# Kernel tuning notes

Measured on AMD Instinct MI355X. Metric: run time of the kernel, lower is better.

Reference implementation:

```python
import jax, jax.numpy as jnp
import numpy as np

B, S, DIM, N, D = 1, 2688, 1536, 12, 128
C = D // 2  # 64 complex pairs per head
EPS = 1e-06


def rms_norm(x, g, eps=EPS):
    # x: [B, S, DIM] -- norm over full model dim, as in WanRMSNorm
    xf = x.astype(jnp.float32)
    return (xf * jax.lax.rsqrt(jnp.mean(xf * xf, axis=-1, keepdims=True) + eps)) * g


def rope_apply(x, f, h, w, freqs_c):
    # x: [B, S, N, D]; freqs_c: complex64 [1024, C]; f*h*w == S (full-seq case)
    s1 = C - 2 * (C // 3)  # 22 (temporal)
    s2 = C // 3            # 21 (height), 21 (width)
    ff = freqs_c[:f, :s1]
    fh = freqs_c[:h, s1:s1 + s2]
    fw = freqs_c[:w, s1 + s2:]
    fi = jnp.concatenate([
        jnp.broadcast_to(ff[:, None, None, :], (f, h, w, s1)),
        jnp.broadcast_to(fh[None, :, None, :], (f, h, w, s2)),
        jnp.broadcast_to(fw[None, None, :, :], (f, h, w, s2)),
    ], axis=-1).reshape(f * h * w, 1, C)  # [S, 1, C]
    xr = x.astype(jnp.float32).reshape(B, S, N, C, 2)
    xc = jax.lax.complex(xr[..., 0], xr[..., 1])          # [B, S, N, C]
    out = xc * fi[None]                                    # broadcast over B, N
    return jnp.stack([out.real, out.imag], axis=-1).reshape(B, S, N, D)


def setup_inputs() -> dict:
    key = jax.random.key(0)
    ks = jax.random.split(key, 12)
    w_scale = 0.02
    # deterministic rope angles (faithful structure: exp(i*theta) per axis slice)
    pos = np.arange(1024, dtype=np.float32)
    inv = 1.0 / (10000.0 ** (np.arange(C, dtype=np.float32) / C))
    ang = pos[:, None] * inv[None, :]
    return {
        "x": jax.random.normal(ks[0], (B, S, DIM), jnp.float32),
        "seq_lens": jnp.full((B,), S, dtype=jnp.int32),
        "grid_sizes": jnp.array([[6, 16, 28]], dtype=jnp.int32),
        "freqs_cos": jnp.asarray(np.cos(ang), jnp.float32),
        "freqs_sin": jnp.asarray(np.sin(ang), jnp.float32),
        "Wq": jax.random.normal(ks[1], (DIM, DIM), jnp.float32) * w_scale,
        "bq": jnp.zeros((DIM,), jnp.float32),
        "Wk": jax.random.normal(ks[2], (DIM, DIM), jnp.float32) * w_scale,
        "bk": jnp.zeros((DIM,), jnp.float32),
        "Wv": jax.random.normal(ks[3], (DIM, DIM), jnp.float32) * w_scale,
        "bv": jnp.zeros((DIM,), jnp.float32),
        "Wo": jax.random.normal(ks[4], (DIM, DIM), jnp.float32) * w_scale,
        "bo": jnp.zeros((DIM,), jnp.float32),
        "gq": jnp.ones((DIM,), jnp.float32),
        "gk": jnp.ones((DIM,), jnp.float32),
    }


def reference(x, seq_lens, grid_sizes, freqs_cos, freqs_sin,
              Wq, bq, Wk, bk, Wv, bv, Wo, bo, gq, gk):
    f, h, w = (int(grid_sizes[0, 0]), int(grid_sizes[0, 1]), int(grid_sizes[0, 2]))
    freqs_c = jax.lax.complex(freqs_cos, freqs_sin)  # [1024, C]

    q = rms_norm(x @ Wq.T + bq, gq).reshape(B, S, N, D)
    k = rms_norm(x @ Wk.T + bk, gk).reshape(B, S, N, D)
    v = (x @ Wv.T + bv).reshape(B, S, N, D)

    q = rope_apply(q, f, h, w, freqs_c)
    k = rope_apply(k, f, h, w, freqs_c)

    # SDPA with key-length masking (k_lens)
    scale = 1.0 / jnp.sqrt(jnp.float32(D))
    scores = jnp.einsum("bqnd,bknd->bnqk", q, k) * scale  # [B, N, S, S]
    kmask = jnp.arange(S)[None, :] < seq_lens[:, None]     # [B, S]
    scores = jnp.where(kmask[:, None, None, :], scores, -jnp.inf)
    attn = jax.nn.softmax(scores, axis=-1)
    out = jnp.einsum("bnqk,bknd->bqnd", attn, v).reshape(B, S, DIM)
    return out @ Wo.T + bo
```

## Files before the change

### kernel.cpp

```cpp
#include <hip/hip_runtime.h>
#include <hip/hip_bf16.h>
#include <stdint.h>

#define S_LEN 2688
#define DIM   1536
#define NH    12
#define HD    128
#define QKV_N 4608

typedef __attribute__((ext_vector_type(8))) short bf16x8;
typedef __attribute__((ext_vector_type(4))) float f32x4;

__device__ inline ushort f2bf(float f) {
    uint32_t u = __float_as_uint(f);
    uint32_t r = (u + 0x7fffu + ((u >> 16) & 1u)) >> 16;
    return (ushort)r;
}
__device__ inline float bf2f(uint u) { return __uint_as_float(u << 16); }
__device__ inline float fexp2(float x) {
    float r;
    asm("v_exp_f32 %0, %1" : "=v"(r) : "v"(x));
    return r;
}
__device__ inline uint cvtpk(float lo, float hi) {
    uint r;
    asm("v_cvt_pk_bf16_f32 %0, %1, %2" : "=v"(r) : "v"(lo), "v"(hi));
    return r;
}

#define GLOAD16(gp, lp) __builtin_amdgcn_global_load_lds( \
    (__attribute__((address_space(1))) const void*)(gp),  \
    (__attribute__((address_space(3))) void*)(lp), 16, 0, 0)

__global__ __launch_bounds__(256) void convert_all(
    const float* __restrict__ x,
    const float* __restrict__ wq, const float* __restrict__ wk,
    const float* __restrict__ wv, const float* __restrict__ wo,
    ushort* __restrict__ xb, ushort* __restrict__ wb)
{
    const size_t NX4 = (size_t)S_LEN * DIM / 4;
    const size_t NW4 = (size_t)DIM * DIM / 4;
    size_t i = (size_t)blockIdx.x * 256 + threadIdx.x;
    const float* src; ushort* dst;
    if (i < NX4)            { src = x;  dst = xb; }
    else if (i < NX4+1*NW4) { src = wq; dst = wb;                        i -= NX4; }
    else if (i < NX4+2*NW4) { src = wk; dst = wb + 1*(size_t)DIM*DIM;    i -= NX4+1*NW4; }
    else if (i < NX4+3*NW4) { src = wv; dst = wb + 2*(size_t)DIM*DIM;    i -= NX4+2*NW4; }
    else if (i < NX4+4*NW4) { src = wo; dst = wb + 3*(size_t)DIM*DIM;    i -= NX4+3*NW4; }
    else return;
    float4 v = reinterpret_cast<const float4*>(src)[i];
    ushort4 o = { f2bf(v.x), f2bf(v.y), f2bf(v.z), f2bf(v.w) };
    reinterpret_cast<ushort4*>(dst)[i] = o;
}

__global__ __launch_bounds__(256) void gemm_qkv(
    const ushort* __restrict__ A, const ushort* __restrict__ B,
    const float* __restrict__ bq, const float* __restrict__ bk,
    const float* __restrict__ bv,
    ushort* __restrict__ qkb, ushort* __restrict__ v_t, int K)
{
    __shared__ ushort At[128 * 64];
    __shared__ ushort Bt[128 * 64];
    const int tid  = threadIdx.x;
    const int wave = tid >> 6, lane = tid & 63;
    const int lid  = blockIdx.y * 21 + blockIdx.x;
    const int xcd  = lid & 7, pos = lid >> 3;
    const int wgid = (xcd < 4 ? xcd * 95 : 4 * 95 + (xcd - 4) * 94) + pos;
    const int m0 = (wgid % 21) * 128, n0 = (wgid / 21) * 128;
    const int wr = wave >> 1, wc = wave & 1;
    const int r = lane & 15, g = lane >> 4;
    const int srow = wave * 8 + (lane >> 3);
    const int scol = (lane & 7) * 8;

    f32x4 acc[4][4] = {};

    for (int k0 = 0; k0 < K; k0 += 64) {
        const ushort* Ag = A + (size_t)m0 * K + k0;
        const ushort* Bg = B + (size_t)n0 * K + k0;
#pragma unroll
        for (int t = 0; t < 4; ++t) {
            GLOAD16(Ag + (size_t)(t*32 + srow) * K + scol, &At[t*2048 + wave*512]);
            GLOAD16(Bg + (size_t)(t*32 + srow) * K + scol, &Bt[t*2048 + wave*512]);
        }
        asm volatile("s_waitcnt vmcnt(0)" ::: "memory");
        __syncthreads();
#pragma unroll
        for (int kk = 0; kk < 2; ++kk) {
            bf16x8 af[4], bfr[4];
#pragma unroll
            for (int i = 0; i < 4; ++i)
                af[i] = *reinterpret_cast<const bf16x8*>(
                    &At[(wr*64 + i*16 + r) * 64 + kk*32 + g*8]);
#pragma unroll
            for (int i = 0; i < 4; ++i)
                bfr[i] = *reinterpret_cast<const bf16x8*>(
                    &Bt[(wc*64 + i*16 + r) * 64 + kk*32 + g*8]);
#pragma unroll
            for (int mi = 0; mi < 4; ++mi)
#pragma unroll
                for (int ni = 0; ni < 4; ++ni)
                    acc[mi][ni] = __builtin_amdgcn_mfma_f32_16x16x32_bf16(
                        af[mi], bfr[ni], acc[mi][ni], 0, 0, 0);
        }
        __syncthreads();
    }

    if (n0 < 2*DIM) {
#pragma unroll
        for (int ni = 0; ni < 4; ++ni) {
            int col = n0 + wc*64 + ni*16 + r;
            float bias = (col < DIM) ? bq[col] : bk[col - DIM];
#pragma unroll
            for (int mi = 0; mi < 4; ++mi) {
                int row = m0 + wr*64 + mi*16 + g*4;
#pragma unroll
                for (int j = 0; j < 4; ++j)
                    qkb[(size_t)(row + j) * (2*DIM) + col] =
                        f2bf(acc[mi][ni][j] + bias);
            }
        }
    } else {
#pragma unroll
        for (int ni = 0; ni < 4; ++ni) {
            int d = n0 - 2*DIM + wc*64 + ni*16 + r;
            float bias = bv[d];
#pragma unroll
            for (int mi = 0; mi < 4; ++mi) {
                int row = m0 + wr*64 + mi*16 + g*4;
                uint2 pkt;
                pkt.x = cvtpk(acc[mi][ni][0] + bias, acc[mi][ni][1] + bias);
                pkt.y = cvtpk(acc[mi][ni][2] + bias, acc[mi][ni][3] + bias);
                *reinterpret_cast<uint2*>(&v_t[(size_t)d * S_LEN + row]) = pkt;
            }
        }
    }
}

__global__ __launch_bounds__(256) void gemm_bt2(
    const ushort* __restrict__ A, const ushort* __restrict__ B,
    const float* __restrict__ b0,
    float* __restrict__ C, int M, int N, int K)
{
    __shared__ ushort At[128 * 64];
    __shared__ ushort Bt[64 * 64];
    const int tid  = threadIdx.x;
    const int wave = tid >> 6, lane = tid & 63;
    const int m0 = blockIdx.x * 128, n0 = blockIdx.y * 64;
    const int wr = wave >> 1, wc = wave & 1;
    const int r = lane & 15, g = lane >> 4;
    const int srow = wave * 8 + (lane >> 3);
    const int scol = (lane & 7) * 8;
    const int brow[2] = { (0*256+tid)>>3, (1*256+tid)>>3 };
    const int bcol = (tid & 7) * 8;

    f32x4 acc[4][2] = {};

    for (int k0 = 0; k0 < K; k0 += 64) {
        const ushort* Ag = A + (size_t)m0 * K + k0;
        const ushort* Bg = B + (size_t)n0 * K + k0;
#pragma unroll
        for (int t = 0; t < 4; ++t)
            GLOAD16(Ag + (size_t)(t*32 + srow) * K + scol, &At[t*2048 + wave*512]);
#pragma unroll
        for (int t = 0; t < 2; ++t)
            GLOAD16(Bg + (size_t)brow[t] * K + bcol, &Bt[(t*256 + wave*64) * 8]);
        asm volatile("s_waitcnt vmcnt(0)" ::: "memory");
        __syncthreads();
#pragma unroll
        for (int kk = 0; kk < 2; ++kk) {
            bf16x8 af[4], bfr[2];
#pragma unroll
            for (int i = 0; i < 4; ++i)
                af[i] = *reinterpret_cast<const bf16x8*>(
                    &At[(wr*64 + i*16 + r) * 64 + kk*32 + g*8]);
#pragma unroll
            for (int i = 0; i < 2; ++i)
                bfr[i] = *reinterpret_cast<const bf16x8*>(
                    &Bt[(wc*32 + i*16 + r) * 64 + kk*32 + g*8]);
#pragma unroll
            for (int mi = 0; mi < 4; ++mi)
#pragma unroll
                for (int ni = 0; ni < 2; ++ni)
                    acc[mi][ni] = __builtin_amdgcn_mfma_f32_16x16x32_bf16(
                        af[mi], bfr[ni], acc[mi][ni], 0, 0, 0);
        }
        __syncthreads();
    }

#pragma unroll
    for (int ni = 0; ni < 2; ++ni) {
        int col = n0 + wc*32 + ni*16 + r;
        float bias = b0[col];
#pragma unroll
        for (int mi = 0; mi < 4; ++mi) {
            int row = m0 + wr*64 + mi*16 + g*4;
#pragma unroll
            for (int j = 0; j < 4; ++j)
                C[(size_t)(row + j) * N + col] = acc[mi][ni][j] + bias;
        }
    }
}

__global__ __launch_bounds__(256) void normrope(
    const ushort* __restrict__ qkb, const int* __restrict__ gsz,
    const float* __restrict__ gq, const float* __restrict__ gk,
    const float* __restrict__ fcos, const float* __restrict__ fsin,
    ushort* __restrict__ q_r, ushort* __restrict__ k_r)
{
    const int s   = blockIdx.x;
    const int tid = threadIdx.x;
    const int wave = tid >> 6, lane = tid & 63;
    const uint* qrow = reinterpret_cast<const uint*>(qkb + (size_t)s * (2*DIM));
    const uint* krow = qrow + DIM/2;

    float2 qv[3], kv[3];
    float sq = 0.f, sk = 0.f;
#pragma unroll
    for (int i = 0; i < 3; ++i) {
        int p = tid + i*256;
        uint uq = qrow[p], uk = krow[p];
        qv[i].x = bf2f(uq & 0xffffu); qv[i].y = bf2f(uq >> 16);
        kv[i].x = bf2f(uk & 0xffffu); kv[i].y = bf2f(uk >> 16);
        sq += qv[i].x*qv[i].x + qv[i].y*qv[i].y;
        sk += kv[i].x*kv[i].x + kv[i].y*kv[i].y;
    }
#pragma unroll
    for (int off = 1; off < 64; off <<= 1) {
        sq += __shfl_xor(sq, off);
        sk += __shfl_xor(sk, off);
    }
    __shared__ float red[4][2];
    if (lane == 0) { red[wave][0] = sq; red[wave][1] = sk; }
    __syncthreads();
    sq = red[0][0] + red[1][0] + red[2][0] + red[3][0];
    sk = red[0][1] + red[1][1] + red[2][1] + red[3][1];
    const float rmsq = rsqrtf(sq * (1.f/DIM) + 1e-6f);
    const float rmsk = rsqrtf(sk * (1.f/DIM) + 1e-6f);

    const int hh = gsz[1], ww = gsz[2];
    const int fidx = s / (hh*ww), rem = s % (hh*ww);
    const int hidx = rem / ww,  widx = rem % ww;
    const float qscale = rmsq * (0.08838834764831845f * 1.4426950408889634f);

#pragma unroll
    for (int i = 0; i < 3; ++i) {
        int p = tid + i*256;
        int c = p & 63, head = p >> 6;
        int coord = (c < 22) ? fidx : (c < 43) ? hidx : widx;
        float cv = fcos[coord*64 + c], sv = fsin[coord*64 + c];
        float2 gqv = reinterpret_cast<const float2*>(gq)[p];
        float2 gkv = reinterpret_cast<const float2*>(gk)[p];
        float a = qv[i].x * qscale * gqv.x, b = qv[i].y * qscale * gqv.y;
        uint qo = cvtpk(a*cv - b*sv, a*sv + b*cv);
        a = kv[i].x * rmsk * gkv.x; b = kv[i].y * rmsk * gkv.y;
        uint ko = cvtpk(a*cv - b*sv, a*sv + b*cv);
        size_t off = (((size_t)head * S_LEN + s) * HD + 2*c) >> 1;
        reinterpret_cast<uint*>(q_r)[off] = qo;
        reinterpret_cast<uint*>(k_r)[off] = ko;
    }
}

__global__ __launch_bounds__(256) void attn_fwd(
    const ushort* __restrict__ q_r, const ushort* __restrict__ k_r,
    const ushort* __restrict__ v_t, const int* __restrict__ seq_lens,
    ushort* __restrict__ attn_out)
{
    __shared__ ushort Kl[2][64 * 128];
    __shared__ ushort Vl[2][128 * 64];
    __shared__ ushort Pl[4][16 * 72];
    const int tid  = threadIdx.x;
    const int wave = tid >> 6, lane = tid & 63;
    const int n  = blockIdx.y;
    const int q0 = blockIdx.x * 64 + wave * 16;
    const int seq = seq_lens[0];
    const int r = lane & 15, g = lane >> 4;
    const int swz = r & 7;
    const ushort* Qh = q_r + (size_t)n * S_LEN * HD;
    const ushort* Kh = k_r + (size_t)n * S_LEN * HD;
    const ushort* Vh = v_t + (size_t)n * HD * S_LEN;

    const int kj_row[4] = { (0*256+tid)>>4, (1*256+tid)>>4, (2*256+tid)>>4, (3*256+tid)>>4 };
    const int kj_w  = tid & 15;
    const int vj_d[4]  = { (0*256+tid)>>3, (1*256+tid)>>3, (2*256+tid)>>3, (3*256+tid)>>3 };
    const int vj_w  = tid & 7;

    bf16x8 qf[4];
#pragma unroll
    for (int c = 0; c < 4; ++c)
        qf[c] = *reinterpret_cast<const bf16x8*>(Qh + (size_t)(q0 + r) * HD + c*32 + g*8);

    f32x4 oacc[8] = {};
    float mrun = -1e30f, lrun = 0.f;

    const int nt = (seq + 63) >> 6;

#define STAGE(buf, kbase)                                                     \
    do {                                                                      \
        _Pragma("unroll")                                                     \
        for (int t = 0; t < 4; ++t) {                                         \
            int row = kj_row[t];                                              \
            GLOAD16(Kh + (size_t)((kbase) + row) * HD + ((kj_w ^ (row & 7)) * 8), \
                    &Kl[buf][(t*256 + wave*64) * 8]);                         \
        }                                                                     \
        _Pragma("unroll")                                                     \
        for (int t = 0; t < 4; ++t) {                                         \
            int d = vj_d[t];                                                  \
            GLOAD16(Vh + (size_t)d * S_LEN + (kbase) + ((vj_w ^ (d & 7)) * 8), \
                    &Vl[buf][(t*256 + wave*64) * 8]);                         \
        }                                                                     \
    } while (0)

    STAGE(0, 0);
    asm volatile("s_waitcnt vmcnt(0)" ::: "memory");
    __syncthreads();

    int cur = 0;
    for (int kt = 0; kt < nt; ++kt) {
        const int k0 = kt * 64;
        if (kt + 1 < nt) STAGE(cur ^ 1, k0 + 64);

        f32x4 sf[4];
#pragma unroll
        for (int kb = 0; kb < 4; ++kb) {
            f32x4 s = {0.f, 0.f, 0.f, 0.f};
            const ushort* kl = &Kl[cur][(kb*16 + r) * 128];
#pragma unroll
            for (int c = 0; c < 4; ++c)
                s = __builtin_amdgcn_mfma_f32_16x16x32_bf16(
                    *reinterpret_cast<const bf16x8*>(kl + ((4*c + g) ^ swz) * 8),
                    qf[c], s, 0, 0, 0);
            sf[kb] = s;
        }
        if (k0 + 64 > seq) {
#pragma unroll
            for (int kb = 0; kb < 4; ++kb)
#pragma unroll
                for (int j = 0; j < 4; ++j)
                    if (k0 + kb*16 + g*4 + j >= seq) sf[kb][j] = -1e30f;
        }
        float pm = fmaxf(fmaxf(fmaxf(sf[0][0], sf[0][1]), fmaxf(sf[0][2], sf[0][3])),
                         fmaxf(fmaxf(sf[1][0], sf[1][1]), fmaxf(sf[1][2], sf[1][3])));
        pm = fmaxf(pm, fmaxf(fmaxf(fmaxf(sf[2][0], sf[2][1]), fmaxf(sf[2][2], sf[2][3])),
                             fmaxf(fmaxf(sf[3][0], sf[3][1]), fmaxf(sf[3][2], sf[3][3]))));
        pm = fmaxf(pm, __shfl_xor(pm, 16));
        pm = fmaxf(pm, __shfl_xor(pm, 32));
        if (!__all(pm - mrun <= 8.f)) {
            float mn = fmaxf(mrun, pm);
            float scl = fexp2(mrun - mn);
            mrun = mn;
            lrun *= scl;
#pragma unroll
            for (int f = 0; f < 8; ++f)
#pragma unroll
                for (int j = 0; j < 4; ++j) oacc[f][j] *= scl;
        }
        float ps = 0.f;
#pragma unroll
        for (int kb = 0; kb < 4; ++kb) {
            float e0 = fexp2(sf[kb][0] - mrun), e1 = fexp2(sf[kb][1] - mrun);
            float e2 = fexp2(sf[kb][2] - mrun), e3 = fexp2(sf[kb][3] - mrun);
            sf[kb][0] = e0; sf[kb][1] = e1; sf[kb][2] = e2; sf[kb][3] = e3;
            ps += (e0 + e1) + (e2 + e3);
        }
        ps += __shfl_xor(ps, 16);
        ps += __shfl_xor(ps, 32);
        lrun += ps;
#pragma unroll
        for (int kb = 0; kb < 4; ++kb) {
            uint2 pkt;
            pkt.x = cvtpk(sf[kb][0], sf[kb][1]);
            pkt.y = cvtpk(sf[kb][2], sf[kb][3]);
            *reinterpret_cast<uint2*>(&Pl[wave][r*72 + kb*16 + g*4]) = pkt;
        }
        bf16x8 pf[2];
        pf[0] = *reinterpret_cast<const bf16x8*>(&Pl[wave][r*72 + g*8]);
        pf[1] = *reinterpret_cast<const bf16x8*>(&Pl[wave][r*72 + 32 + g*8]);
#pragma unroll
        for (int db = 0; db < 8; ++db) {
            const ushort* vl = &Vl[cur][(db*16 + r) * 64];
#pragma unroll
            for (int kb2 = 0; kb2 < 2; ++kb2)
                oacc[db] = __builtin_amdgcn_mfma_f32_16x16x32_bf16(
                    *reinterpret_cast<const bf16x8*>(vl + ((kb2*4 + g) ^ swz) * 8),
                    pf[kb2], oacc[db], 0, 0, 0);
        }

        if (kt + 1 < nt) {
            asm volatile("s_waitcnt vmcnt(0)" ::: "memory");
            __syncthreads();
            cur ^= 1;
        }
    }
#undef STAGE

    const float inv = (lrun > 0.f) ? 1.f / lrun : 0.f;
#pragma unroll
    for (int db = 0; db < 8; ++db) {
        uint2 pkt;
        pkt.x = cvtpk(oacc[db][0]*inv, oacc[db][1]*inv);
        pkt.y = cvtpk(oacc[db][2]*inv, oacc[db][3]*inv);
        *reinterpret_cast<uint2*>(
            &attn_out[(size_t)(q0 + r) * DIM + n*HD + db*16 + g*4]) = pkt;
    }
}

extern "C" void kernel_launch(void* const* d_in, const int* in_sizes, int n_in,
                              void* d_out, int out_size, void* d_ws, size_t ws_size,
                              hipStream_t stream)
{
    const float* x    = (const float*)d_in[0];
    const int*   seqL = (const int*)  d_in[1];
    const int*   gsz  = (const int*)  d_in[2];
    const float* fcos = (const float*)d_in[3];
    const float* fsin = (const float*)d_in[4];
    const float* Wq   = (const float*)d_in[5];
    const float* bq   = (const float*)d_in[6];
    const float* Wk   = (const float*)d_in[7];
    const float* bk   = (const float*)d_in[8];
    const float* Wv   = (const float*)d_in[9];
    const float* bv   = (const float*)d_in[10];
    const float* Wo   = (const float*)d_in[11];
    const float* bo   = (const float*)d_in[12];
    const float* gq   = (const float*)d_in[13];
    const float* gk   = (const float*)d_in[14];
    float* out = (float*)d_out;

    char* ws = (char*)d_ws;
    ushort* xb  = (ushort*)ws;
    ushort* wb  = xb  + (size_t)S_LEN * DIM;
    ushort* qkb = wb  + 4*(size_t)DIM*DIM;
    ushort* v_t = qkb + (size_t)S_LEN * 2*DIM;
    ushort* q_r = v_t + (size_t)DIM * S_LEN;
    ushort* k_r = q_r + (size_t)S_LEN * DIM;
    ushort* ao  = k_r + (size_t)S_LEN * DIM;

    convert_all<<<13248, 256, 0, stream>>>(x, Wq, Wk, Wv, Wo, xb, wb);
    gemm_qkv<<<dim3(21, 36), 256, 0, stream>>>(xb, wb, bq, bk, bv,
                                               qkb, v_t, DIM);
    normrope<<<S_LEN, 256, 0, stream>>>(qkb, gsz, gq, gk, fcos, fsin, q_r, k_r);
    attn_fwd<<<dim3(42, 12), 256, 0, stream>>>(q_r, k_r, v_t, seqL, ao);
    gemm_bt2<<<dim3(21, 24), 256, 0, stream>>>(ao, wb + 3*(size_t)DIM*DIM,
                                               bo, out, S_LEN, DIM, DIM);
}
```

Before: 216.9 us.

## Use 32x32x16 MFMA with split-K waves and permlane P exchange

Reworks the attention kernel so each wave pair shares 32 query rows. Each wave of the pair handles one 32-key half of every 64-key tile using 32x32x16 bf16 MFMAs. The P tile is rearranged in registers with v_permlane32_swap instead of a round trip through LDS. The two halves' softmax states and output accumulators are merged through shared memory at the end. This cuts LDS traffic and the count of MFMA instructions, at the cost of a final cross-wave reduction and larger per-thread register use.

Result: faster. 208.8 us (-3.8%).

```diff
diff --git a/kernel.cpp b/kernel.cpp
--- a/kernel.cpp
+++ b/kernel.cpp
@@ -8,8 +8,9 @@
 #define HD    128
 #define QKV_N 4608
 
-typedef __attribute__((ext_vector_type(8))) short bf16x8;
-typedef __attribute__((ext_vector_type(4))) float f32x4;
+typedef __attribute__((ext_vector_type(8)))  short bf16x8;
+typedef __attribute__((ext_vector_type(4)))  float f32x4;
+typedef __attribute__((ext_vector_type(16))) float f32x16;
 
 __device__ inline ushort f2bf(float f) {
     uint32_t u = __float_as_uint(f);
@@ -267,14 +268,13 @@
 {
     __shared__ ushort Kl[2][64 * 128];
     __shared__ ushort Vl[2][128 * 64];
-    __shared__ ushort Pl[4][16 * 72];
     const int tid  = threadIdx.x;
     const int wave = tid >> 6, lane = tid & 63;
     const int n  = blockIdx.y;
-    const int q0 = blockIdx.x * 64 + wave * 16;
     const int seq = seq_lens[0];
-    const int r = lane & 15, g = lane >> 4;
-    const int swz = r & 7;
+    const int khalf = wave & 1, pair = wave >> 1;
+    const int ql = lane & 31, h = lane >> 5, sw = lane & 7;
+    const int qrow = blockIdx.x * 64 + pair * 32 + ql;
     const ushort* Qh = q_r + (size_t)n * S_LEN * HD;
     const ushort* Kh = k_r + (size_t)n * S_LEN * HD;
     const ushort* Vh = v_t + (size_t)n * HD * S_LEN;
@@ -284,12 +284,12 @@
     const int vj_d[4]  = { (0*256+tid)>>3, (1*256+tid)>>3, (2*256+tid)>>3, (3*256+tid)>>3 };
     const int vj_w  = tid & 7;
 
-    bf16x8 qf[4];
-#pragma unroll
-    for (int c = 0; c < 4; ++c)
-        qf[c] = *reinterpret_cast<const bf16x8*>(Qh + (size_t)(q0 + r) * HD + c*32 + g*8);
-
-    f32x4 oacc[8] = {};
+    bf16x8 qf[8];
+#pragma unroll
+    for (int c = 0; c < 8; ++c)
+        qf[c] = *reinterpret_cast<const bf16x8*>(Qh + (size_t)qrow * HD + c*16 + h*8);
+
+    f32x16 oacc[4] = {};
     float mrun = -1e30f, lrun = 0.f;
 
     const int nt = (seq + 63) >> 6;
@@ -316,33 +316,24 @@
 
     int cur = 0;
     for (int kt = 0; kt < nt; ++kt) {
-        const int k0 = kt * 64;
-        if (kt + 1 < nt) STAGE(cur ^ 1, k0 + 64);
-
-        f32x4 sf[4];
-#pragma unroll
-        for (int kb = 0; kb < 4; ++kb) {
-            f32x4 s = {0.f, 0.f, 0.f, 0.f};
-            const ushort* kl = &Kl[cur][(kb*16 + r) * 128];
-#pragma unroll
-            for (int c = 0; c < 4; ++c)
-                s = __builtin_amdgcn_mfma_f32_16x16x32_bf16(
-                    *reinterpret_cast<const bf16x8*>(kl + ((4*c + g) ^ swz) * 8),
-                    qf[c], s, 0, 0, 0);
-            sf[kb] = s;
-        }
-        if (k0 + 64 > seq) {
-#pragma unroll
-            for (int kb = 0; kb < 4; ++kb)
-#pragma unroll
-                for (int j = 0; j < 4; ++j)
-                    if (k0 + kb*16 + g*4 + j >= seq) sf[kb][j] = -1e30f;
-        }
-        float pm = fmaxf(fmaxf(fmaxf(sf[0][0], sf[0][1]), fmaxf(sf[0][2], sf[0][3])),
-                         fmaxf(fmaxf(sf[1][0], sf[1][1]), fmaxf(sf[1][2], sf[1][3])));
-        pm = fmaxf(pm, fmaxf(fmaxf(fmaxf(sf[2][0], sf[2][1]), fmaxf(sf[2][2], sf[2][3])),
-                             fmaxf(fmaxf(sf[3][0], sf[3][1]), fmaxf(sf[3][2], sf[3][3]))));
-        pm = fmaxf(pm, __shfl_xor(pm, 16));
+        const int k0 = kt * 64 + khalf * 32;
+        if (kt + 1 < nt) STAGE(cur ^ 1, (kt+1) * 64);
+
+        f32x16 sf = {};
+        const ushort* kl = &Kl[cur][(khalf*32 + ql) * 128];
+#pragma unroll
+        for (int c = 0; c < 8; ++c)
+            sf = __builtin_amdgcn_mfma_f32_32x32x16_bf16(
+                *reinterpret_cast<const bf16x8*>(kl + ((2*c + h) ^ sw) * 8),
+                qf[c], sf, 0, 0, 0);
+        if (k0 + 32 > seq) {
+#pragma unroll
+            for (int j = 0; j < 16; ++j)
+                if (k0 + (j&3) + 8*(j>>2) + 4*h >= seq) sf[j] = -1e30f;
+        }
+        float pm = sf[0];
+#pragma unroll
+        for (int j = 1; j < 16; ++j) pm = fmaxf(pm, sf[j]);
         pm = fmaxf(pm, __shfl_xor(pm, 32));
         if (!__all(pm - mrun <= 8.f)) {
             float mn = fmaxf(mrun, pm);
@@ -350,39 +341,39 @@
             mrun = mn;
             lrun *= scl;
 #pragma unroll
-            for (int f = 0; f < 8; ++f)
-#pragma unroll
-                for (int j = 0; j < 4; ++j) oacc[f][j] *= scl;
+            for (int db = 0; db < 4; ++db)
+#pragma unroll
+                for (int j = 0; j < 16; ++j) oacc[db][j] *= scl;
         }
         float ps = 0.f;
 #pragma unroll
-        for (int kb = 0; kb < 4; ++kb) {
-            float e0 = fexp2(sf[kb][0] - mrun), e1 = fexp2(sf[kb][1] - mrun);
-            float e2 = fexp2(sf[kb][2] - mrun), e3 = fexp2(sf[kb][3] - mrun);
-            sf[kb][0] = e0; sf[kb][1] = e1; sf[kb][2] = e2; sf[kb][3] = e3;
-            ps += (e0 + e1) + (e2 + e3);
-        }
-        ps += __shfl_xor(ps, 16);
+        for (int j = 0; j < 16; ++j) {
+            float e = fexp2(sf[j] - mrun);
+            sf[j] = e;
+            ps += e;
+        }
         ps += __shfl_xor(ps, 32);
         lrun += ps;
-#pragma unroll
-        for (int kb = 0; kb < 4; ++kb) {
-            uint2 pkt;
-            pkt.x = cvtpk(sf[kb][0], sf[kb][1]);
-            pkt.y = cvtpk(sf[kb][2], sf[kb][3]);
-            *reinterpret_cast<uint2*>(&Pl[wave][r*72 + kb*16 + g*4]) = pkt;
-        }
-        bf16x8 pf[2];
-        pf[0] = *reinterpret_cast<const bf16x8*>(&Pl[wave][r*72 + g*8]);
-        pf[1] = *reinterpret_cast<const bf16x8*>(&Pl[wave][r*72 + 32 + g*8]);
-#pragma unroll
-        for (int db = 0; db < 8; ++db) {
-            const ushort* vl = &Vl[cur][(db*16 + r) * 64];
-#pragma unroll
-            for (int kb2 = 0; kb2 < 2; ++kb2)
-                oacc[db] = __builtin_amdgcn_mfma_f32_16x16x32_bf16(
-                    *reinterpret_cast<const bf16x8*>(vl + ((kb2*4 + g) ^ swz) * 8),
-                    pf[kb2], oacc[db], 0, 0, 0);
+        uint u0 = cvtpk(sf[0],  sf[1]),  u1 = cvtpk(sf[2],  sf[3]);
+        uint u2 = cvtpk(sf[4],  sf[5]),  u3 = cvtpk(sf[6],  sf[7]);
+        uint u4 = cvtpk(sf[8],  sf[9]),  u5 = cvtpk(sf[10], sf[11]);
+        uint u6 = cvtpk(sf[12], sf[13]), u7 = cvtpk(sf[14], sf[15]);
+        asm("v_permlane32_swap_b32 %0, %1" : "+v"(u0), "+v"(u2));
+        asm("v_permlane32_swap_b32 %0, %1" : "+v"(u1), "+v"(u3));
+        asm("v_permlane32_swap_b32 %0, %1" : "+v"(u4), "+v"(u6));
+        asm("v_permlane32_swap_b32 %0, %1" : "+v"(u5), "+v"(u7));
+        union { uint uu[4]; bf16x8 v; } fa, fb;
+        fa.uu[0] = u0; fa.uu[1] = u1; fa.uu[2] = u2; fa.uu[3] = u3;
+        fb.uu[0] = u4; fb.uu[1] = u5; fb.uu[2] = u6; fb.uu[3] = u7;
+#pragma unroll
+        for (int db = 0; db < 4; ++db) {
+            const ushort* vl = &Vl[cur][(db*32 + ql) * 64];
+            oacc[db] = __builtin_amdgcn_mfma_f32_32x32x16_bf16(
+                *reinterpret_cast<const bf16x8*>(vl + ((khalf*4 + 0 + h) ^ sw) * 8),
+                fa.v, oacc[db], 0, 0, 0);
+            oacc[db] = __builtin_amdgcn_mfma_f32_32x32x16_bf16(
+                *reinterpret_cast<const bf16x8*>(vl + ((khalf*4 + 2 + h) ^ sw) * 8),
+                fb.v, oacc[db], 0, 0, 0);
         }
 
         if (kt + 1 < nt) {
@@ -393,14 +384,44 @@
     }
 #undef STAGE
 
-    const float inv = (lrun > 0.f) ? 1.f / lrun : 0.f;
-#pragma unroll
-    for (int db = 0; db < 8; ++db) {
-        uint2 pkt;
-        pkt.x = cvtpk(oacc[db][0]*inv, oacc[db][1]*inv);
-        pkt.y = cvtpk(oacc[db][2]*inv, oacc[db][3]*inv);
-        *reinterpret_cast<uint2*>(
-            &attn_out[(size_t)(q0 + r) * DIM + n*HD + db*16 + g*4]) = pkt;
+    __syncthreads();
+    float* Obuf  = (float*)&Kl[0][0];
+    float* MLbuf = (float*)&Vl[0][0];
+    if (khalf == 1) {
+#pragma unroll
+        for (int db = 0; db < 4; ++db)
+#pragma unroll
+            for (int j = 0; j < 16; ++j) {
+                int d = db*32 + (j&3) + 8*(j>>2) + 4*h;
+                Obuf[pair*4096 + d*32 + ql] = oacc[db][j];
+            }
+        if (h == 0) { MLbuf[pair*64 + ql] = mrun; MLbuf[pair*64 + 32 + ql] = lrun; }
+    }
+    __syncthreads();
+    if (khalf == 0) {
+        float m2 = MLbuf[pair*64 + ql], l2 = MLbuf[pair*64 + 32 + ql];
+        float mm = fmaxf(mrun, m2);
+        float s1 = fexp2(mrun - mm), s2 = fexp2(m2 - mm);
+        float ltot = lrun * s1 + l2 * s2;
+        float inv = (ltot > 0.f) ? 1.f / ltot : 0.f;
+#pragma unroll
+        for (int db = 0; db < 4; ++db)
+#pragma unroll
+            for (int j = 0; j < 16; ++j) {
+                int d = db*32 + (j&3) + 8*(j>>2) + 4*h;
+                oacc[db][j] = (oacc[db][j] * s1 +
+                               Obuf[pair*4096 + d*32 + ql] * s2) * inv;
+            }
+#pragma unroll
+        for (int db = 0; db < 4; ++db)
+#pragma unroll
+            for (int jg = 0; jg < 4; ++jg) {
+                uint2 pkt;
+                pkt.x = cvtpk(oacc[db][jg*4+0], oacc[db][jg*4+1]);
+                pkt.y = cvtpk(oacc[db][jg*4+2], oacc[db][jg*4+3]);
+                *reinterpret_cast<uint2*>(
+                    &attn_out[(size_t)qrow * DIM + n*HD + db*32 + jg*8 + 4*h]) = pkt;
+            }
     }
 }
 
```
